# Optimization experiments

Measured on AMD Instinct MI355X. Metric: run time of the kernel, lower is better.

The kernel has to match this reference:

```python
import jax, jax.numpy as jnp
import numpy as np

DIM = 384; HEADS = 6; POINTS = 4; LEVELS = 3; HID = 96
B = 2; D0 = 12; H0 = 12; W0 = 12
NMID = D0 * H0 * W0          # mid-level tokens
NTOK = 73 * NMID // 8        # total tokens across 3 scales


def _ln(x, w, b, eps=1e-6):
    m = x.mean(-1, keepdims=True)
    v = ((x - m) ** 2).mean(-1, keepdims=True)
    return (x - m) * jax.lax.rsqrt(v + eps) * w + b


def _make_ref(shapes):
    # matches get_reference_points: per-level normalized centers, stacked as (d, x, y)
    refs = []
    for (D_, H_, W_) in shapes:
        d = (jnp.arange(D_, dtype=jnp.float32) + 0.5) / D_
        y = (jnp.arange(H_, dtype=jnp.float32) + 0.5) / H_
        x = (jnp.arange(W_, dtype=jnp.float32) + 0.5) / W_
        dd, yy, xx = jnp.meshgrid(d, y, x, indexing='ij')
        refs.append(jnp.stack([dd.ravel(), xx.ravel(), yy.ravel()], -1))
    return jnp.concatenate(refs, 0)[None, :, None, :]  # [1, N, 1, 3]


def _sample_level(v, D_, H_, W_, loc):
    # v: [B,S,h,hd]; loc: [B,Nq,h,P,3] normalized (d,x,y); trilinear, zero padding,
    # align_corners=False semantics (pixel = norm*size - 0.5)
    Bq, Nq, h, P, _ = loc.shape
    hd = v.shape[-1]
    pd = loc[..., 0] * D_ - 0.5
    px = loc[..., 1] * W_ - 0.5
    py = loc[..., 2] * H_ - 0.5
    d0 = jnp.floor(pd); x0 = jnp.floor(px); y0 = jnp.floor(py)
    fd = pd - d0; fx = px - x0; fy = py - y0
    d0 = d0.astype(jnp.int32); x0 = x0.astype(jnp.int32); y0 = y0.astype(jnp.int32)
    acc = jnp.zeros((Bq, Nq, h, P, hd), v.dtype)
    for dd in (0, 1):  # fixed 8-corner loop
        for dy in (0, 1):
            for dx in (0, 1):
                di = d0 + dd; yi = y0 + dy; xi = x0 + dx
                wgt = (fd if dd else 1.0 - fd) * (fy if dy else 1.0 - fy) * (fx if dx else 1.0 - fx)
                valid = ((di >= 0) & (di < D_) & (yi >= 0) & (yi < H_) & (xi >= 0) & (xi < W_)).astype(v.dtype)
                idx = (jnp.clip(di, 0, D_ - 1) * H_ + jnp.clip(yi, 0, H_ - 1)) * W_ + jnp.clip(xi, 0, W_ - 1)
                idx_t = idx.transpose(0, 1, 3, 2).reshape(Bq, Nq * P, h)
                g = jnp.take_along_axis(v, idx_t[..., None], axis=1)  # [B,Nq*P,h,hd]
                g = g.reshape(Bq, Nq, P, h, hd).transpose(0, 1, 3, 2, 4)
                acc = acc + (wgt * valid)[..., None] * g
    return acc  # [B,Nq,h,P,hd]


def _msdeform(q, ref, feat, shapes, off_w, off_b, aw_w, aw_b, val_w, val_b, out_w, out_b):
    Bq, Nq, C = q.shape
    hd = C // HEADS
    value = (feat @ val_w + val_b).reshape(Bq, -1, HEADS, hd)
    off = (q @ off_w + off_b).reshape(Bq, Nq, HEADS, LEVELS, POINTS, 3)
    aw = jax.nn.softmax((q @ aw_w + aw_b).reshape(Bq, Nq, HEADS, LEVELS * POINTS), -1)
    aw = aw.reshape(Bq, Nq, HEADS, LEVELS, POINTS)
    # offset normalizer in (d, x, y) order -> (D, W, H)
    norm = jnp.array([[D_, W_, H_] for (D_, H_, W_) in shapes], dtype=q.dtype)
    loc = ref[:, :, None, :, None, :] + off / norm[None, None, None, :, None, :]
    out = jnp.zeros((Bq, Nq, HEADS, hd), q.dtype)
    start = 0
    for l, (D_, H_, W_) in enumerate(shapes):
        S = D_ * H_ * W_
        sampled = _sample_level(value[:, start:start + S], D_, H_, W_, loc[:, :, :, l])
        out = out + jnp.einsum('bqhp,bqhpd->bqhd', aw[:, :, :, l], sampled)
        start += S
    return out.reshape(Bq, Nq, C) @ out_w + out_b


def _dwconv_seg(x, Dv, Hv, Wv, w, b):
    Bq, S, C = x.shape
    xv = x.reshape(Bq, Dv, Hv, Wv, C)
    y = jax.lax.conv_general_dilated(xv, w, (1, 1, 1), 'SAME',
                                     dimension_numbers=('NDHWC', 'DHWIO', 'NDHWC'),
                                     feature_group_count=C) + b
    return y.reshape(Bq, S, C)


def _conv_ffn(x, D, H, W, fc1_w, fc1_b, dw_w, dw_b, fc2_w, fc2_b):
    x = x @ fc1_w + fc1_b
    n = x.shape[1] // 73
    x1 = _dwconv_seg(x[:, :64 * n], 2 * D, 2 * H, 2 * W, dw_w, dw_b)
    x2 = _dwconv_seg(x[:, 64 * n:72 * n], D, H, W, dw_w, dw_b)
    x3 = _dwconv_seg(x[:, 72 * n:], D // 2, H // 2, W // 2, dw_w, dw_b)
    x = jax.nn.gelu(jnp.concatenate([x1, x2, x3], 1), approximate=False)
    return x @ fc2_w + fc2_b


def _forward(query, feat, D, H, W,
             qnorm_w, qnorm_b, fnorm_w, fnorm_b, ext_qnorm_w, ext_qnorm_b,
             ext_fnorm_w, ext_fnorm_b, ffn_norm_w, ffn_norm_b,
             off_w, off_b, aw_w, aw_b, val_w, val_b, out_w, out_b,
             fc1_w, fc1_b, dw_w, dw_b, fc2_w, fc2_b):
    n_mid = D * H * W
    n_high = 8 * n_mid
    x2 = query[:, n_high:n_high + n_mid] + feat
    q = jnp.concatenate([query[:, :n_high], x2, query[:, n_high + n_mid:]], 1)
    shapes = [(2 * D, 2 * H, 2 * W), (D, H, W), (D // 2, H // 2, W // 2)]
    ref = _make_ref(shapes)
    qn = _ln(q, qnorm_w, qnorm_b)      # CTI_toC.query_norm
    fn = _ln(q, fnorm_w, fnorm_b)      # CTI_toC.feat_norm
    aq = _ln(qn, ext_qnorm_w, ext_qnorm_b)  # MultiscaleExtractor.query_norm
    af = _ln(fn, ext_fnorm_w, ext_fnorm_b)  # MultiscaleExtractor.feat_norm
    out = qn + _msdeform(aq, ref, af, shapes, off_w, off_b, aw_w, aw_b, val_w, val_b, out_w, out_b)
    out = out + _conv_ffn(_ln(out, ffn_norm_w, ffn_norm_b), D, H, W,
                          fc1_w, fc1_b, dw_w, dw_b, fc2_w, fc2_b)
    return out


def setup_inputs() -> dict:
    key = jax.random.key(0)
    ks = jax.random.split(key, 16)
    w = lambda k, *s: jax.random.normal(k, s, jnp.float32) * 0.02
    NO = HEADS * LEVELS * POINTS * 3
    NA = HEADS * LEVELS * POINTS
    return {
        'query': jax.random.normal(ks[0], (B, NTOK, DIM), jnp.float32),
        'reference_points': jax.random.uniform(ks[1], (1, NTOK, 1, 3), dtype=jnp.float32),
        'feat': jax.random.normal(ks[2], (B, NMID, DIM), jnp.float32),
        'spatial_shapes': jnp.array([[2 * D0, 2 * H0, 2 * W0], [D0, H0, W0], [D0 // 2, H0 // 2, W0 // 2]], jnp.int32),
        'level_start_index': jnp.array([0, 8 * NMID, 9 * NMID], jnp.int32),
        'D': D0, 'H': H0, 'W': W0,
        'qnorm_w': jnp.ones(DIM), 'qnorm_b': jnp.zeros(DIM),
        'fnorm_w': jnp.ones(DIM), 'fnorm_b': jnp.zeros(DIM),
        'ext_qnorm_w': jnp.ones(DIM), 'ext_qnorm_b': jnp.zeros(DIM),
        'ext_fnorm_w': jnp.ones(DIM), 'ext_fnorm_b': jnp.zeros(DIM),
        'ffn_norm_w': jnp.ones(DIM), 'ffn_norm_b': jnp.zeros(DIM),
        'off_w': w(ks[3], DIM, NO), 'off_b': jnp.zeros(NO),
        'aw_w': w(ks[4], DIM, NA), 'aw_b': jnp.zeros(NA),
        'val_w': w(ks[5], DIM, DIM), 'val_b': jnp.zeros(DIM),
        'out_w': w(ks[6], DIM, DIM), 'out_b': jnp.zeros(DIM),
        'fc1_w': w(ks[7], DIM, HID), 'fc1_b': jnp.zeros(HID),
        'dw_w': w(ks[8], 3, 3, 3, 1, HID), 'dw_b': jnp.zeros(HID),
        'fc2_w': w(ks[9], HID, DIM), 'fc2_b': jnp.zeros(DIM),
    }


def reference(query, reference_points, feat, spatial_shapes, level_start_index, D, H, W,
              qnorm_w, qnorm_b, fnorm_w, fnorm_b, ext_qnorm_w, ext_qnorm_b,
              ext_fnorm_w, ext_fnorm_b, ffn_norm_w, ffn_norm_b,
              off_w, off_b, aw_w, aw_b, val_w, val_b, out_w, out_b,
              fc1_w, fc1_b, dw_w, dw_b, fc2_w, fc2_b):
    # reference_points / spatial_shapes / level_start_index are required by the torch
    # signature but unused: CTI_toC recomputes deform inputs internally.
    return _forward(query, feat, D, H, W,
                    qnorm_w, qnorm_b, fnorm_w, fnorm_b, ext_qnorm_w, ext_qnorm_b,
                    ext_fnorm_w, ext_fnorm_b, ffn_norm_w, ffn_norm_b,
                    off_w, off_b, aw_w, aw_b, val_w, val_b, out_w, out_b,
                    fc1_w, fc1_b, dw_w, dw_b, fc2_w, fc2_b)
```

## Files before the change

kernel.cpp:

```cpp
#include <hip/hip_runtime.h>
#include <hip/hip_fp16.h>
#include <cstdint>
#include <cstddef>

#define DIM    384
#define HEADS  6
#define HD     64
#define NTOK   15768
#define NMID   1728
#define BATCH  2
#define ROWS   (BATCH*NTOK)
#define MPAD   31616
#define L1START 13824
#define L2START 15552
#define HID    96
#define VROWS  (ROWS + 8)
#define VSLAB  ((size_t)VROWS * 64)

typedef __attribute__((ext_vector_type(8))) short short8;
typedef __attribute__((ext_vector_type(4))) float floatx4;

__device__ __forceinline__ unsigned short f2bf(float x){
  unsigned u = __float_as_uint(x);
  unsigned r = (u + 0x7FFFu + ((u >> 16) & 1u)) >> 16;
  return (unsigned short)r;
}

__device__ __forceinline__ float wave_sum(float v){
  #pragma unroll
  for (int o = 32; o; o >>= 1) v += __shfl_xor(v, o, 64);
  return v;
}

__device__ __forceinline__ void ln384(const float* x, float* y,
                                      const float* __restrict__ w,
                                      const float* __restrict__ b, int lane){
  float s = 0.f;
  #pragma unroll
  for (int j = 0; j < 6; j++) s += x[j];
  s = wave_sum(s);
  float m = s * (1.f/384.f);
  float v = 0.f;
  #pragma unroll
  for (int j = 0; j < 6; j++){ float d = x[j] - m; v += d*d; }
  v = wave_sum(v) * (1.f/384.f);
  float rs = rsqrtf(v + 1e-6f);
  #pragma unroll
  for (int j = 0; j < 6; j++){
    int c = j*64 + lane;
    y[j] = (x[j] - m) * rs * w[c] + b[c];
  }
}

__global__ void k_ln_front(const float* __restrict__ query, const float* __restrict__ feat,
                           const float* __restrict__ qw,  const float* __restrict__ qb,
                           const float* __restrict__ fw,  const float* __restrict__ fb,
                           const float* __restrict__ eqw, const float* __restrict__ eqb,
                           const float* __restrict__ efw, const float* __restrict__ efb,
                           float* __restrict__ qn, unsigned short* __restrict__ aq,
                           unsigned short* __restrict__ af){
  int wid = blockIdx.x * (blockDim.x >> 6) + (threadIdx.x >> 6);
  if (wid >= ROWS) return;
  int lane = threadIdx.x & 63;
  int b = wid / NTOK, t = wid - b*NTOK;
  const float* qp = query + (size_t)wid * DIM;
  float x[6];
  #pragma unroll
  for (int j = 0; j < 6; j++) x[j] = qp[j*64 + lane];
  if (t >= L1START && t < L2START){
    const float* fp = feat + ((size_t)b*NMID + (t - L1START)) * DIM;
    #pragma unroll
    for (int j = 0; j < 6; j++) x[j] += fp[j*64 + lane];
  }
  float y[6], z[6];
  ln384(x, y, qw, qb, lane);
  {
    float* o = qn + (size_t)wid * DIM;
    #pragma unroll
    for (int j = 0; j < 6; j++) o[j*64 + lane] = y[j];
  }
  ln384(y, z, eqw, eqb, lane);
  {
    unsigned short* o = aq + (size_t)wid * DIM;
    #pragma unroll
    for (int j = 0; j < 6; j++) o[j*64 + lane] = f2bf(z[j]);
  }
  ln384(x, y, fw, fb, lane);
  ln384(y, z, efw, efb, lane);
  {
    unsigned short* o = af + (size_t)wid * DIM;
    #pragma unroll
    for (int j = 0; j < 6; j++) o[j*64 + lane] = f2bf(z[j]);
  }
}

__global__ void k_ln(const float* __restrict__ in, const float* __restrict__ w,
                     const float* __restrict__ b, unsigned short* __restrict__ out){
  int wid = blockIdx.x * (blockDim.x >> 6) + (threadIdx.x >> 6);
  if (wid >= ROWS) return;
  int lane = threadIdx.x & 63;
  float x[6], y[6];
  const float* p = in + (size_t)wid * DIM;
  #pragma unroll
  for (int j = 0; j < 6; j++) x[j] = p[j*64 + lane];
  ln384(x, y, w, b, lane);
  unsigned short* o = out + (size_t)wid * DIM;
  #pragma unroll
  for (int j = 0; j < 6; j++) o[j*64 + lane] = f2bf(y[j]);
}

__global__ void k_cvt_all(const float* __restrict__ val_w, const float* __restrict__ off_w,
                          const float* __restrict__ aw_w,  const float* __restrict__ out_w,
                          const float* __restrict__ fc1_w, const float* __restrict__ fc2_w,
                          const float* __restrict__ off_b, const float* __restrict__ aw_b,
                          unsigned short* __restrict__ wt_val, unsigned short* __restrict__ wt_offaw,
                          unsigned short* __restrict__ wt_out, unsigned short* __restrict__ wt_fc1,
                          unsigned short* __restrict__ wt_fc2, float* __restrict__ offaw_b){
  int id = blockIdx.x * blockDim.x + threadIdx.x;
  if (id < 147456){
    int n = id / 384, k = id - n*384;
    wt_val[id] = f2bf(val_w[(size_t)k*384 + n]);
  } else if (id < 294912){
    int i = id - 147456;
    int n = i / 384, k = i - n*384;
    float v = 0.f;
    if (n < 216) v = off_w[(size_t)k*216 + n];
    else if (n >= 256 && n < 328) v = aw_w[(size_t)k*72 + (n-256)];
    wt_offaw[i] = f2bf(v);
  } else if (id < 442368){
    int i = id - 294912;
    int n = i / 384, k = i - n*384;
    wt_out[i] = f2bf(out_w[(size_t)k*384 + n]);
  } else if (id < 491520){
    int i = id - 442368;
    int n = i / 384, k = i - n*384;
    wt_fc1[i] = f2bf((n < 96) ? fc1_w[(size_t)k*96 + n] : 0.f);
  } else if (id < 528384){
    int i = id - 491520;
    int n = i / 96, k = i - n*96;
    wt_fc2[i] = f2bf(fc2_w[(size_t)k*384 + n]);
  } else if (id < 528768){
    int n = id - 528384;
    float v = 0.f;
    if (n < 216) v = off_b[n];
    else if (n >= 256 && n < 328) v = aw_b[n-256];
    offaw_b[n] = v;
  }
}

template<int OUTMODE>
__global__ __launch_bounds__(256) void k_gemm(
    const unsigned short* __restrict__ A,
    const unsigned short* __restrict__ Wt,
    const float* __restrict__ bias,
    const float* __restrict__ R,
    void* __restrict__ Cv,
    int M, int N, int K){
  __shared__ __align__(16) unsigned short As[128*32];
  __shared__ __align__(16) unsigned short Bs[128*32];
  int tid = threadIdx.x;
  int w = tid >> 6, lane = tid & 63;
  int m0 = blockIdx.y * 128, n0 = blockIdx.x * 128;
  int m_off = (w & 1) * 64, n_off = (w >> 1) * 64;

  floatx4 acc[4][4] = {};

  int sr = lane >> 2;
  int sc = (lane & 3) * 8;
  int lrow = lane & 15;
  int kq = (lane >> 4) * 8;

  for (int k0 = 0; k0 < K; k0 += 32){
    #pragma unroll
    for (int s = 0; s < 2; s++){
      int c = w * 2 + s;
      const unsigned short* ga = A  + (size_t)(m0 + c*16 + sr) * K + k0 + sc;
      __builtin_amdgcn_global_load_lds(
          (const __attribute__((address_space(1))) void*)ga,
          (__attribute__((address_space(3))) void*)(As + c*512), 16, 0, 0);
      const unsigned short* gb = Wt + (size_t)(n0 + c*16 + sr) * K + k0 + sc;
      __builtin_amdgcn_global_load_lds(
          (const __attribute__((address_space(1))) void*)gb,
          (__attribute__((address_space(3))) void*)(Bs + c*512), 16, 0, 0);
    }
    __syncthreads();
    short8 afr[4], bfr[4];
    #pragma unroll
    for (int i = 0; i < 4; i++)
      afr[i] = *(const short8*)(As + (m_off + i*16 + lrow)*32 + kq);
    #pragma unroll
    for (int j = 0; j < 4; j++)
      bfr[j] = *(const short8*)(Bs + (n_off + j*16 + lrow)*32 + kq);
    #pragma unroll
    for (int i = 0; i < 4; i++)
      #pragma unroll
      for (int j = 0; j < 4; j++)
        acc[i][j] = __builtin_amdgcn_mfma_f32_16x16x32_bf16(afr[i], bfr[j], acc[i][j], 0, 0, 0);
    __syncthreads();
  }

  int cn = n0 + n_off + lrow;
  int rbase = m0 + m_off + (lane >> 4) * 4;
  #pragma unroll
  for (int j = 0; j < 4; j++){
    int n = cn + j*16;
    if (n >= N) continue;
    float bj = bias[n];
    #pragma unroll
    for (int i = 0; i < 4; i++){
      int mb = rbase + i*16;
      #pragma unroll
      for (int r = 0; r < 4; r++){
        int m = mb + r;
        if (m < M){
          float v = acc[i][j][r] + bj;
          if (R) v += R[(size_t)m * N + n];
          if (OUTMODE == 0)      ((float*)Cv)[(size_t)m * N + n] = v;
          else if (OUTMODE == 1) ((unsigned short*)Cv)[(size_t)m * N + n] = f2bf(v);
          else {
            ((__half*)Cv)[(size_t)(n >> 6) * VSLAB + (size_t)m * 64 + (n & 63)] =
                __float2half_rn(v);
          }
        }
      }
    }
  }
}

__global__ __launch_bounds__(384) void k_msdeform(const __half* __restrict__ vt,
                                                  const float* __restrict__ offaw,
                                                  unsigned short* __restrict__ msout){
  int bx = blockIdx.x;
  int r = (bx & 7) * (ROWS/8) + (bx >> 3);
  int head = threadIdx.x >> 6;
  int lane = threadIdx.x & 63;
  int b = (r >= NTOK) ? 1 : 0;
  int t = r - b * NTOK;

  float refd, refy, refx;
  if (t < L1START){
    int i = t;
    int dd = i / 576; int rem = i - dd*576; int yy = rem / 24; int xx = rem - yy*24;
    refd = (dd + 0.5f) * (1.f/24.f); refy = (yy + 0.5f) * (1.f/24.f); refx = (xx + 0.5f) * (1.f/24.f);
  } else if (t < L2START){
    int i = t - L1START;
    int dd = i / 144; int rem = i - dd*144; int yy = rem / 12; int xx = rem - yy*12;
    refd = (dd + 0.5f) * (1.f/12.f); refy = (yy + 0.5f) * (1.f/12.f); refx = (xx + 0.5f) * (1.f/12.f);
  } else {
    int i = t - L2START;
    int dd = i / 36; int rem = i - dd*36; int yy = rem / 6; int xx = rem - yy*6;
    refd = (dd + 0.5f) * (1.f/6.f); refy = (yy + 0.5f) * (1.f/6.f); refx = (xx + 0.5f) * (1.f/6.f);
  }

  float logit = (lane < 12) ? offaw[(size_t)r * 384 + 256 + head * 12 + lane] : -1e30f;
  float mx = logit;
  mx = fmaxf(mx, __shfl_xor(mx, 1));
  mx = fmaxf(mx, __shfl_xor(mx, 2));
  mx = fmaxf(mx, __shfl_xor(mx, 4));
  mx = fmaxf(mx, __shfl_xor(mx, 8));
  float e = (lane < 12) ? __expf(logit - mx) : 0.f;
  float s = e;
  s += __shfl_xor(s, 1);
  s += __shfl_xor(s, 2);
  s += __shfl_xor(s, 4);
  s += __shfl_xor(s, 8);
  float aww = e / s;
  float awwj = __shfl(aww, lane >> 2, 64);

  int rowk = 0, wgtk = 0;
  if (lane < 48){
    int j = lane >> 2, p = lane & 3;
    int l = j >> 2;
    int Dl  = (l == 0) ? 24 : ((l == 1) ? 12 : 6);
    int lst = (l == 0) ? 0  : ((l == 1) ? L1START : L2START);
    const float* op = offaw + (size_t)r * 384 + head * 36 + j * 3;
    float od = op[0], ox = op[1], oy = op[2];
    float fDl = (float)Dl;
    float pd = refd * fDl + od - 0.5f;
    float px = refx * fDl + ox - 0.5f;
    float py = refy * fDl + oy - 0.5f;
    float fld = floorf(pd), flx = floorf(px), fly = floorf(py);
    float fd = pd - fld, fx = px - flx, fy = py - fly;
    int d0 = (int)fld, x0 = (int)flx, y0 = (int)fly;
    int cz = p >> 1, cy = p & 1;
    int di = d0 + cz, yi = y0 + cy;
    bool vzy = (di >= 0) & (di < Dl) & (yi >= 0) & (yi < Dl);
    float wz = cz ? fd : 1.f - fd;
    float wy = cy ? fy : 1.f - fy;
    float wp = vzy ? (wz * awwj) * wy : 0.f;
    int rs = min(max(x0, 0), Dl - 1);
    float wlo_x = (rs == x0) ? (1.f - fx) : ((rs == x0 + 1) ? fx : 0.f);
    float whi_x = ((rs == x0) && (x0 + 1 < Dl)) ? fx : 0.f;
    int dc = min(max(di, 0), Dl - 1);
    int yc = min(max(yi, 0), Dl - 1);
    rowk = (b * NTOK + lst) + (dc * Dl + yc) * Dl + rs;
    __half2 wh = __floats2half2_rn(wp * wlo_x, wp * whi_x);
    wgtk = *(int*)&wh;
  }

  int head_u = __builtin_amdgcn_readfirstlane(head);
  const char* vbase = (const char*)(vt + (size_t)head_u * VSLAB);
  unsigned lane4 = (unsigned)lane << 2;
  unsigned selperm = (lane & 32) ? 0x03020302u : 0x01000100u;

  __half2 hz; *(int*)&hz = 0;
  __half2 a0 = hz, a1 = hz, a2 = hz, a3 = hz;
  float fLo = 0.f, fHi = 0.f;

  #pragma unroll
  for (int seg = 0; seg < 3; seg++){
    #pragma unroll
    for (int q = 0; q < 4; q++){
      int kb = seg * 16 + q * 4;
      int s0 = __builtin_amdgcn_readlane(rowk, kb + 0);
      int s1 = __builtin_amdgcn_readlane(rowk, kb + 1);
      int s2 = __builtin_amdgcn_readlane(rowk, kb + 2);
      int s3 = __builtin_amdgcn_readlane(rowk, kb + 3);
      int sw0 = __builtin_amdgcn_readlane(wgtk, kb + 0);
      int sw1 = __builtin_amdgcn_readlane(wgtk, kb + 1);
      int sw2 = __builtin_amdgcn_readlane(wgtk, kb + 2);
      int sw3 = __builtin_amdgcn_readlane(wgtk, kb + 3);
      unsigned o0 = (((unsigned)s0) << 7) + lane4;
      unsigned o1 = (((unsigned)s1) << 7) + lane4;
      unsigned o2 = (((unsigned)s2) << 7) + lane4;
      unsigned o3 = (((unsigned)s3) << 7) + lane4;
      __half2 v0 = *(const __half2*)(vbase + o0);
      __half2 v1 = *(const __half2*)(vbase + o1);
      __half2 v2 = *(const __half2*)(vbase + o2);
      __half2 v3 = *(const __half2*)(vbase + o3);
      unsigned u0 = __builtin_amdgcn_perm((unsigned)sw0, (unsigned)sw0, selperm);
      unsigned u1 = __builtin_amdgcn_perm((unsigned)sw1, (unsigned)sw1, selperm);
      unsigned u2 = __builtin_amdgcn_perm((unsigned)sw2, (unsigned)sw2, selperm);
      unsigned u3 = __builtin_amdgcn_perm((unsigned)sw3, (unsigned)sw3, selperm);
      a0 = __hfma2(*(__half2*)&u0, v0, a0);
      a1 = __hfma2(*(__half2*)&u1, v1, a1);
      a2 = __hfma2(*(__half2*)&u2, v2, a2);
      a3 = __hfma2(*(__half2*)&u3, v3, a3);
    }
    float2 f0 = __half22float2(a0), f1 = __half22float2(a1);
    float2 f2 = __half22float2(a2), f3 = __half22float2(a3);
    fLo += (f0.x + f1.x) + (f2.x + f3.x);
    fHi += (f0.y + f1.y) + (f2.y + f3.y);
    a0 = a1 = a2 = a3 = hz;
  }

  float sLo = fLo + __shfl_xor(fLo, 32);
  float sHi = fHi + __shfl_xor(fHi, 32);
  if (lane < 32){
    unsigned packed = ((unsigned)f2bf(sHi) << 16) | (unsigned)f2bf(sLo);
    *(unsigned*)(msout + (size_t)r * DIM + head * 64 + lane * 2) = packed;
  }
}

__global__ void k_dwconv_gelu(const float* __restrict__ h, const float* __restrict__ dww,
                              const float* __restrict__ dwb, unsigned short* __restrict__ h2){
  int gid = blockIdx.x * blockDim.x + threadIdx.x;
  if (gid >= ROWS * 24) return;
  int c4 = gid % 24;
  int r = gid / 24;
  int c = c4 * 4;
  int b = (r >= NTOK) ? 1 : 0;
  int t = r - b * NTOK;
  int base, DL, i;
  if (t < L1START){ base = 0; DL = 24; i = t; }
  else if (t < L2START){ base = L1START; DL = 12; i = t - L1START; }
  else { base = L2START; DL = 6; i = t - L2START; }
  int dd, yy, xx;
  if (DL == 24){ dd = i / 576; int rem = i - dd*576; yy = rem / 24; xx = rem - yy*24; }
  else if (DL == 12){ dd = i / 144; int rem = i - dd*144; yy = rem / 12; xx = rem - yy*12; }
  else { dd = i / 36; int rem = i - dd*36; yy = rem / 6; xx = rem - yy*6; }
  float4 acc = {0.f, 0.f, 0.f, 0.f};
  #pragma unroll
  for (int kz = 0; kz < 3; kz++){
    int nd = dd + kz - 1; if (nd < 0 || nd >= DL) continue;
    #pragma unroll
    for (int ky = 0; ky < 3; ky++){
      int ny = yy + ky - 1; if (ny < 0 || ny >= DL) continue;
      #pragma unroll
      for (int kx = 0; kx < 3; kx++){
        int nx = xx + kx - 1; if (nx < 0 || nx >= DL) continue;
        int nt = base + (nd * DL + ny) * DL + nx;
        float4 hv = *(const float4*)(h + ((size_t)(b*NTOK + nt)) * HID + c);
        float4 wv = *(const float4*)(dww + (size_t)((kz*3 + ky)*3 + kx) * HID + c);
        acc.x += hv.x * wv.x; acc.y += hv.y * wv.y;
        acc.z += hv.z * wv.z; acc.w += hv.w * wv.w;
      }
    }
  }
  float4 bv = *(const float4*)(dwb + c);
  acc.x += bv.x; acc.y += bv.y; acc.z += bv.z; acc.w += bv.w;
  const float k = 0.70710678118654752440f;
  float g0 = 0.5f * acc.x * (1.f + erff(acc.x * k));
  float g1 = 0.5f * acc.y * (1.f + erff(acc.y * k));
  float g2 = 0.5f * acc.z * (1.f + erff(acc.z * k));
  float g3 = 0.5f * acc.w * (1.f + erff(acc.w * k));
  uint2 pk;
  pk.x = ((unsigned)f2bf(g1) << 16) | (unsigned)f2bf(g0);
  pk.y = ((unsigned)f2bf(g3) << 16) | (unsigned)f2bf(g2);
  *(uint2*)(h2 + (size_t)r * HID + c) = pk;
}

extern "C" void kernel_launch(void* const* d_in, const int* in_sizes, int n_in,
                              void* d_out, int out_size, void* d_ws, size_t ws_size,
                              hipStream_t stream){
  const float* query = (const float*)d_in[0];
  const float* feat  = (const float*)d_in[2];
  const float* qnw = (const float*)d_in[8],  *qnb = (const float*)d_in[9];
  const float* fnw = (const float*)d_in[10], *fnb = (const float*)d_in[11];
  const float* eqw = (const float*)d_in[12], *eqb = (const float*)d_in[13];
  const float* efw = (const float*)d_in[14], *efb = (const float*)d_in[15];
  const float* ffw = (const float*)d_in[16], *ffb = (const float*)d_in[17];
  const float* off_w = (const float*)d_in[18], *off_b = (const float*)d_in[19];
  const float* aw_w  = (const float*)d_in[20], *aw_b  = (const float*)d_in[21];
  const float* val_w = (const float*)d_in[22], *val_b = (const float*)d_in[23];
  const float* out_w = (const float*)d_in[24], *out_b = (const float*)d_in[25];
  const float* fc1_w = (const float*)d_in[26], *fc1_b = (const float*)d_in[27];
  const float* dw_w  = (const float*)d_in[28], *dw_b  = (const float*)d_in[29];
  const float* fc2_w = (const float*)d_in[30], *fc2_b = (const float*)d_in[31];
  float* out = (float*)d_out;

  char* p = (char*)d_ws;
  float* qn             = (float*)p;          p += (size_t)ROWS*384*4;
  unsigned short* aq    = (unsigned short*)p; p += (size_t)MPAD*384*2;
  unsigned short* af    = (unsigned short*)p; p += (size_t)MPAD*384*2;
  __half* value_t       = (__half*)p;         p += (size_t)HEADS*VSLAB*2;
  float* offaw          = (float*)p;          p += (size_t)ROWS*384*4;
  unsigned short* wt_val   = (unsigned short*)p; p += (size_t)384*384*2;
  unsigned short* wt_offaw = (unsigned short*)p; p += (size_t)384*384*2;
  unsigned short* wt_out   = (unsigned short*)p; p += (size_t)384*384*2;
  unsigned short* wt_fc1   = (unsigned short*)p; p += (size_t)128*384*2;
  unsigned short* wt_fc2   = (unsigned short*)p; p += (size_t)384*96*2;
  float* offaw_b           = (float*)p;          p += (size_t)384*4;
  unsigned short* t_buf  = aq;
  unsigned short* msout  = af;
  float* y1              = offaw;
  float* h_buf           = (float*)value_t;
  unsigned short* h2_buf = (unsigned short*)qn;

  k_cvt_all<<<(528768 + 255)/256, 256, 0, stream>>>(val_w, off_w, aw_w, out_w, fc1_w, fc2_w,
                                                    off_b, aw_b,
                                                    wt_val, wt_offaw, wt_out, wt_fc1, wt_fc2,
                                                    offaw_b);

  int lnBlocks = ROWS / 4;
  k_ln_front<<<lnBlocks, 256, 0, stream>>>(query, feat, qnw, qnb, fnw, fnb,
                                           eqw, eqb, efw, efb, qn, aq, af);

  dim3 gN384(3, MPAD/128), gN128(1, MPAD/128);

  k_gemm<2><<<gN384, 256, 0, stream>>>(af, wt_val, val_b, nullptr, value_t, ROWS, 384, 384);
  k_gemm<0><<<gN384, 256, 0, stream>>>(aq, wt_offaw, offaw_b, nullptr, offaw, ROWS, 384, 384);
  k_msdeform<<<ROWS, 384, 0, stream>>>(value_t, offaw, msout);
  k_gemm<0><<<gN384, 256, 0, stream>>>(msout, wt_out, out_b, qn, y1, ROWS, 384, 384);
  k_ln<<<lnBlocks, 256, 0, stream>>>(y1, ffw, ffb, t_buf);
  k_gemm<0><<<gN128, 256, 0, stream>>>(t_buf, wt_fc1, fc1_b, nullptr, h_buf, ROWS, 96, 384);
  k_dwconv_gelu<<<(ROWS * 24 + 255)/256, 256, 0, stream>>>(h_buf, dw_w, dw_b, h2_buf);
  k_gemm<0><<<gN384, 256, 0, stream>>>(h2_buf, wt_fc2, fc2_b, y1, out, ROWS, 384, 96);
}
```

Baseline: 531.8 us.

## Gather value rows with 16-byte loads across four lane groups in deformable sampling

```diff
diff --git a/kernel.cpp b/kernel.cpp
--- a/kernel.cpp
+++ b/kernel.cpp
@@ -298,57 +298,56 @@
     wgtk = *(int*)&wh;
   }
 
+  int grp = lane >> 4;
+  unsigned selperm = (lane & 8) ? 0x03020302u : 0x01000100u;
+  int rowv[12]; unsigned wsel[12];
+  #pragma unroll
+  for (int j = 0; j < 12; j++){
+    rowv[j] = __shfl(rowk, j*4 + grp, 64);
+    unsigned wj = (unsigned)__shfl(wgtk, j*4 + grp, 64);
+    wsel[j] = __builtin_amdgcn_perm(wj, wj, selperm);
+  }
+
   int head_u = __builtin_amdgcn_readfirstlane(head);
   const char* vbase = (const char*)(vt + (size_t)head_u * VSLAB);
-  unsigned lane4 = (unsigned)lane << 2;
-  unsigned selperm = (lane & 32) ? 0x03020302u : 0x01000100u;
+  unsigned laneoff = (unsigned)(lane & 15) << 4;
 
   __half2 hz; *(int*)&hz = 0;
   __half2 a0 = hz, a1 = hz, a2 = hz, a3 = hz;
-  float fLo = 0.f, fHi = 0.f;
-
-  #pragma unroll
-  for (int seg = 0; seg < 3; seg++){
-    #pragma unroll
-    for (int q = 0; q < 4; q++){
-      int kb = seg * 16 + q * 4;
-      int s0 = __builtin_amdgcn_readlane(rowk, kb + 0);
-      int s1 = __builtin_amdgcn_readlane(rowk, kb + 1);
-      int s2 = __builtin_amdgcn_readlane(rowk, kb + 2);
-      int s3 = __builtin_amdgcn_readlane(rowk, kb + 3);
-      int sw0 = __builtin_amdgcn_readlane(wgtk, kb + 0);
-      int sw1 = __builtin_amdgcn_readlane(wgtk, kb + 1);
-      int sw2 = __builtin_amdgcn_readlane(wgtk, kb + 2);
-      int sw3 = __builtin_amdgcn_readlane(wgtk, kb + 3);
-      unsigned o0 = (((unsigned)s0) << 7) + lane4;
-      unsigned o1 = (((unsigned)s1) << 7) + lane4;
-      unsigned o2 = (((unsigned)s2) << 7) + lane4;
-      unsigned o3 = (((unsigned)s3) << 7) + lane4;
-      __half2 v0 = *(const __half2*)(vbase + o0);
-      __half2 v1 = *(const __half2*)(vbase + o1);
-      __half2 v2 = *(const __half2*)(vbase + o2);
-      __half2 v3 = *(const __half2*)(vbase + o3);
-      unsigned u0 = __builtin_amdgcn_perm((unsigned)sw0, (unsigned)sw0, selperm);
-      unsigned u1 = __builtin_amdgcn_perm((unsigned)sw1, (unsigned)sw1, selperm);
-      unsigned u2 = __builtin_amdgcn_perm((unsigned)sw2, (unsigned)sw2, selperm);
-      unsigned u3 = __builtin_amdgcn_perm((unsigned)sw3, (unsigned)sw3, selperm);
-      a0 = __hfma2(*(__half2*)&u0, v0, a0);
-      a1 = __hfma2(*(__half2*)&u1, v1, a1);
-      a2 = __hfma2(*(__half2*)&u2, v2, a2);
-      a3 = __hfma2(*(__half2*)&u3, v3, a3);
-    }
-    float2 f0 = __half22float2(a0), f1 = __half22float2(a1);
-    float2 f2 = __half22float2(a2), f3 = __half22float2(a3);
-    fLo += (f0.x + f1.x) + (f2.x + f3.x);
-    fHi += (f0.y + f1.y) + (f2.y + f3.y);
-    a0 = a1 = a2 = a3 = hz;
-  }
-
-  float sLo = fLo + __shfl_xor(fLo, 32);
-  float sHi = fHi + __shfl_xor(fHi, 32);
-  if (lane < 32){
-    unsigned packed = ((unsigned)f2bf(sHi) << 16) | (unsigned)f2bf(sLo);
-    *(unsigned*)(msout + (size_t)r * DIM + head * 64 + lane * 2) = packed;
+  #pragma unroll
+  for (int j = 0; j < 12; j++){
+    unsigned off = ((unsigned)rowv[j] << 7) + laneoff;
+    uint4 v = *(const uint4*)(vbase + off);
+    __half2 wh = *(__half2*)&wsel[j];
+    a0 = __hfma2(wh, *(__half2*)&v.x, a0);
+    a1 = __hfma2(wh, *(__half2*)&v.y, a1);
+    a2 = __hfma2(wh, *(__half2*)&v.z, a2);
+    a3 = __hfma2(wh, *(__half2*)&v.w, a3);
+  }
+
+  int i0 = *(int*)&a0, i1 = *(int*)&a1, i2 = *(int*)&a2, i3 = *(int*)&a3;
+  int p0 = __shfl_xor(i0, 8, 64); int p1 = __shfl_xor(i1, 8, 64);
+  int p2 = __shfl_xor(i2, 8, 64); int p3 = __shfl_xor(i3, 8, 64);
+  a0 = __hadd2(a0, *(__half2*)&p0);
+  a1 = __hadd2(a1, *(__half2*)&p1);
+  a2 = __hadd2(a2, *(__half2*)&p2);
+  a3 = __hadd2(a3, *(__half2*)&p3);
+  float2 f0 = __half22float2(a0), f1 = __half22float2(a1);
+  float2 f2 = __half22float2(a2), f3 = __half22float2(a3);
+  float sv[8] = {f0.x, f0.y, f1.x, f1.y, f2.x, f2.y, f3.x, f3.y};
+  #pragma unroll
+  for (int k = 0; k < 8; k++){
+    sv[k] += __shfl_xor(sv[k], 16, 64);
+    sv[k] += __shfl_xor(sv[k], 32, 64);
+  }
+
+  if (lane < 8){
+    uint4 pk;
+    pk.x = ((unsigned)f2bf(sv[1]) << 16) | (unsigned)f2bf(sv[0]);
+    pk.y = ((unsigned)f2bf(sv[3]) << 16) | (unsigned)f2bf(sv[2]);
+    pk.z = ((unsigned)f2bf(sv[5]) << 16) | (unsigned)f2bf(sv[4]);
+    pk.w = ((unsigned)f2bf(sv[7]) << 16) | (unsigned)f2bf(sv[6]);
+    *(uint4*)(msout + (size_t)r * DIM + head * 64 + lane * 8) = pk;
   }
 }
 
```

Result: faster. 511.5 us (-3.8%).
